# Performance work log

Hardware: AMD Instinct MI355X
Metric: run time of the kernel (lower is better)

## Reference

```python
import jax, jax.numpy as jnp
import numpy as np

A = 15                    # num_anchor_per_point
H = W = 34                # hardcoded feature map size in the torch module
STRIDE = 16               # heat_map_a
ANCHOR_W = jnp.array([45.3, 32.0, 22.6, 90.5, 64.0, 45.3, 181.0, 128.0, 90.5, 271.5, 192.0, 135.8, 362.0, 256.0, 181.0], dtype=jnp.float32)
ANCHOR_H = jnp.array([22.6, 32.0, 45.3, 45.3, 64.0, 90.5, 90.5, 128.0, 181.0, 135.8, 192.0, 271.5, 181.0, 256.0, 362.0], dtype=jnp.float32)
THRESH_OBJ = 0.2
MIN_H = 6.0
MIN_W = 6.0
MAX_CAND = 5000
TOP_N = 300
OVERLAP = 0.7


def _generate_anchors():
    xmins = -0.5 * (ANCHOR_W - 1.0)
    xmaxs = 0.5 * (ANCHOR_W - 1.0)
    ymins = -0.5 * (ANCHOR_H - 1.0)
    ymaxs = 0.5 * (ANCHOR_H - 1.0)
    return jnp.stack([xmins, ymins, xmaxs, ymaxs], axis=1)  # [A,4]


def _bbox_transform_inv(boxes, deltas):
    widths = boxes[:, 2] - boxes[:, 0] + 1.0
    heights = boxes[:, 3] - boxes[:, 1] + 1.0
    ctr_x = boxes[:, 0] + 0.5 * (widths - 1.0)
    ctr_y = boxes[:, 1] + 0.5 * (heights - 1.0)
    pred_ctr_x = deltas[:, 0] * widths + ctr_x
    pred_ctr_y = deltas[:, 1] * heights + ctr_y
    pred_w = jnp.exp(deltas[:, 2]) * widths
    pred_h = jnp.exp(deltas[:, 3]) * heights
    return jnp.stack([
        pred_ctr_x - 0.5 * (pred_w - 1.0),
        pred_ctr_y - 0.5 * (pred_h - 1.0),
        pred_ctr_x + 0.5 * (pred_w - 1.0),
        pred_ctr_y + 0.5 * (pred_h - 1.0),
    ], axis=1)


def _nms_keep(boxes, valid, thresh):
    # greedy NMS on score-descending boxes; +1 pixel convention matches module
    x1, y1, x2, y2 = boxes[:, 0], boxes[:, 1], boxes[:, 2], boxes[:, 3]
    areas = (x2 - x1 + 1.0) * (y2 - y1 + 1.0)
    iw = jnp.clip(jnp.minimum(x2[:, None], x2[None, :]) - jnp.maximum(x1[:, None], x1[None, :]) + 1.0, 0.0)
    ih = jnp.clip(jnp.minimum(y2[:, None], y2[None, :]) - jnp.maximum(y1[:, None], y1[None, :]) + 1.0, 0.0)
    inter = iw * ih
    iou = inter / (areas[:, None] + areas[None, :] - inter)  # [M,M]
    M = boxes.shape[0]
    idx = jnp.arange(M)

    def body(i, suppressed):
        alive = jnp.logical_not(suppressed[i])
        return suppressed | (alive & (iou[i] > thresh) & (idx > i))

    suppressed = jax.lax.fori_loop(0, M, body, jnp.logical_not(valid))
    return jnp.logical_not(suppressed) & valid


def _forward(rpn_cls_prob_reshape, rpn_bbox_pred, im_info, bbox_mean, bbox_std):
    origin_height = im_info[0].astype(jnp.float32)
    origin_width = im_info[1].astype(jnp.float32)

    # shifts (replicates torch meshgrid indexing='ij' and (y,x,y,x) column order)
    shift_x = jnp.arange(W, dtype=jnp.float32) * STRIDE
    shift_y = jnp.arange(H, dtype=jnp.float32) * STRIDE
    sx, sy = jnp.meshgrid(shift_x, shift_y, indexing='ij')  # [W,H]
    shifts = jnp.stack([sy.ravel(), sx.ravel(), sy.ravel(), sx.ravel()], axis=1)  # [W*H,4]
    anchors = (_generate_anchors()[None, :, :] + shifts[:, None, :]).reshape(-1, 4)  # [W*H*A,4]

    # deltas: [1,4A,34,34] -> (A,4,34,34) -> (34,34,A,4) -> (-1,4)
    deltas = rpn_bbox_pred.reshape(A, 4, H, W).transpose(2, 3, 0, 1).reshape(-1, 4)
    deltas = deltas * bbox_std + bbox_mean
    proposals = _bbox_transform_inv(anchors, deltas)

    # clip to image (refine_out_of_map_bbox=True)
    xs = jnp.clip(proposals[:, 0::2], 0.0, origin_width - 1.0)
    ys = jnp.clip(proposals[:, 1::2], 0.0, origin_height - 1.0)
    proposals = jnp.stack([xs[:, 0], ys[:, 0], xs[:, 1], ys[:, 1]], axis=1)

    # scores: [1,2A,34,34] -> (2,A,HW) -> (HW,A,2) -> (-1,2)
    scores = rpn_cls_prob_reshape.reshape(2, A, -1).transpose(2, 1, 0).reshape(-1, 2)

    # filter (HEIGHT_AND_WIDTH) via masking (jit-friendly, same selected set)
    ws = proposals[:, 2] - proposals[:, 0] + 1.0
    hs = proposals[:, 3] - proposals[:, 1] + 1.0
    keep = (scores[:, 1] > THRESH_OBJ) & (ws >= MIN_W) & (hs >= MIN_H)

    masked_score = jnp.where(keep, scores[:, 1], -1.0)
    top_vals, top_idx = jax.lax.top_k(masked_score, MAX_CAND)  # sorted descending
    cand = proposals[top_idx]
    valid = keep[top_idx]

    kept = _nms_keep(cand, valid, OVERLAP)

    # emit first TOP_N kept boxes in score order, zero-padded, with batch-id col 0
    rank = jnp.cumsum(kept.astype(jnp.int32)) - 1
    dest = jnp.where(kept & (rank < TOP_N), rank, TOP_N)
    out = jnp.zeros((TOP_N + 1, 5), dtype=cand.dtype)
    out = out.at[dest, 1:].set(cand)
    return out[:TOP_N]


def setup_inputs() -> dict:
    key = jax.random.key(0)
    k1, k2 = jax.random.split(key)
    rpn_cls_prob_reshape = jax.random.uniform(k1, (1, 2 * A, H, W), dtype=jnp.float32)
    rpn_bbox_pred = jax.random.normal(k2, (1, 4 * A, H, W), dtype=jnp.float32)
    im_info = jnp.array([544, 544], dtype=jnp.int32)
    bbox_mean = jnp.array([0.0, 0.0, 0.0, 0.0], dtype=jnp.float32)
    bbox_std = jnp.array([0.1, 0.1, 0.2, 0.2], dtype=jnp.float32)
    return {"rpn_cls_prob_reshape": rpn_cls_prob_reshape, "rpn_bbox_pred": rpn_bbox_pred,
            "im_info": im_info, "bbox_mean": bbox_mean, "bbox_std": bbox_std}


def reference(rpn_cls_prob_reshape, rpn_bbox_pred, im_info, bbox_mean, bbox_std):
    return _forward(rpn_cls_prob_reshape, rpn_bbox_pred, im_info, bbox_mean, bbox_std)
```

## Files before the change

kernel.cpp:

```cpp
#include <hip/hip_runtime.h>

#define NA 15
#define GH 34
#define GW 34
#define SP (GH*GW)
#define NB (SP*NA)
#define MAXC 5000
#define TOPN 300
#define NW 80
#define NRALLOC 5056
#define THRESH_OBJ 0.2f
#define NMS_T 0.7f
#define SH 12
#define BLO 0x3E4CCu
#define NBUCK 5120

typedef unsigned long long u64;
typedef unsigned int u32;
struct __align__(16) U2 { u64 x, y; };

__constant__ float c_aw[NA] = {45.3f,32.0f,22.6f,90.5f,64.0f,45.3f,181.0f,128.0f,90.5f,271.5f,192.0f,135.8f,362.0f,256.0f,181.0f};
__constant__ float c_ah[NA] = {22.6f,32.0f,45.3f,45.3f,64.0f,90.5f,90.5f,128.0f,181.0f,135.8f,192.0f,271.5f,181.0f,256.0f,362.0f};

__global__ __launch_bounds__(256) void k_decode(
    const float* __restrict__ cls, const float* __restrict__ pred,
    const int* __restrict__ iminfo, const float* __restrict__ mean,
    const float* __restrict__ stdv, float* __restrict__ boxes,
    u32* __restrict__ sbits, int* __restrict__ hist) {
#pragma clang fp contract(off)
  int r = blockIdx.x * 256 + threadIdx.x;
  if (r >= NB) return;
  int n = r % NA;
  int p = r / NA;
  int w = p % GW;
  int h = p / GW;

  float score = cls[(NA + n) * SP + p];

  float d0 = pred[(n*4+0)*SP + p] * stdv[0] + mean[0];
  float d1 = pred[(n*4+1)*SP + p] * stdv[1] + mean[1];
  float d2 = pred[(n*4+2)*SP + p] * stdv[2] + mean[2];
  float d3 = pred[(n*4+3)*SP + p] * stdv[3] + mean[3];

  float aw = c_aw[n], ah = c_ah[n];
  float sx = (float)(w * 16);
  float sy = (float)(h * 16);
  float xmin = -0.5f * (aw - 1.0f) + sx;
  float ymin = -0.5f * (ah - 1.0f) + sy;
  float xmax =  0.5f * (aw - 1.0f) + sx;
  float ymax =  0.5f * (ah - 1.0f) + sy;

  float widths  = xmax - xmin + 1.0f;
  float heights = ymax - ymin + 1.0f;
  float ctrx = xmin + 0.5f * (widths - 1.0f);
  float ctry = ymin + 0.5f * (heights - 1.0f);

  float pcx = d0 * widths + ctrx;
  float pcy = d1 * heights + ctry;
  float pw = expf(d2) * widths;
  float ph = expf(d3) * heights;

  float x1 = pcx - 0.5f * (pw - 1.0f);
  float y1 = pcy - 0.5f * (ph - 1.0f);
  float x2 = pcx + 0.5f * (pw - 1.0f);
  float y2 = pcy + 0.5f * (ph - 1.0f);

  float ow = (float)iminfo[1] - 1.0f;
  float oh = (float)iminfo[0] - 1.0f;
  x1 = fminf(fmaxf(x1, 0.0f), ow);
  x2 = fminf(fmaxf(x2, 0.0f), ow);
  y1 = fminf(fmaxf(y1, 0.0f), oh);
  y2 = fminf(fmaxf(y2, 0.0f), oh);

  float ws = x2 - x1 + 1.0f;
  float hs = y2 - y1 + 1.0f;
  bool keep = (score > THRESH_OBJ) && (ws >= 6.0f) && (hs >= 6.0f);

  boxes[r*4+0] = x1;
  boxes[r*4+1] = y1;
  boxes[r*4+2] = x2;
  boxes[r*4+3] = y2;
  u32 bits = keep ? __float_as_uint(score) : 0u;
  sbits[r] = bits;
  if (bits) {
    int b = min((int)((bits >> SH) - BLO), NBUCK - 1);
    atomicAdd(&hist[b], 1);
  }
}

__global__ __launch_bounds__(1024) void k_scan(const int* __restrict__ hist,
    int* __restrict__ base, int* __restrict__ cnt) {
  __shared__ int sh[NBUCK];
  __shared__ int ch[1024];
  int tid = threadIdx.x;
  for (int j = tid; j < NBUCK; j += 1024) sh[j] = hist[j];
  __syncthreads();
  int c0 = sh[tid*5+0], c1 = sh[tid*5+1], c2 = sh[tid*5+2], c3 = sh[tid*5+3], c4 = sh[tid*5+4];
  ch[tid] = c0 + c1 + c2 + c3 + c4;
  __syncthreads();
  for (int off = 1; off < 1024; off <<= 1) {
    int v = ch[tid];
    int u = (tid + off < 1024) ? ch[tid + off] : 0;
    __syncthreads();
    ch[tid] = v + u;
    __syncthreads();
  }
  int S = (tid + 1 < 1024) ? ch[tid + 1] : 0;
  int b4 = S;
  int b3 = b4 + c4;
  int b2 = b3 + c3;
  int b1 = b2 + c2;
  int b0 = b1 + c1;
  base[tid*5+0] = b0; base[tid*5+1] = b1; base[tid*5+2] = b2;
  base[tid*5+3] = b3; base[tid*5+4] = b4;
  if (tid == 0) *cnt = ch[0];
}

__global__ __launch_bounds__(256) void k_place(const u32* __restrict__ sbits,
    const int* __restrict__ base, int* __restrict__ fill, u64* __restrict__ blist) {
  int i = blockIdx.x * 256 + threadIdx.x;
  if (i >= NB) return;
  u32 bits = sbits[i];
  if (!bits) return;
  int b = min((int)((bits >> SH) - BLO), NBUCK - 1);
  int pos = base[b] + atomicAdd(&fill[b], 1);
  blist[pos] = ((u64)bits << 32) | (u64)(0xFFFFFFFFu - (u32)i);
}

__global__ __launch_bounds__(256) void k_final(const u32* __restrict__ sbits,
    const int* __restrict__ base, const int* __restrict__ cnt,
    const u64* __restrict__ blist, const float* __restrict__ boxes,
    float* __restrict__ sboxes) {
  int i = blockIdx.x * 256 + threadIdx.x;
  if (i >= NB) return;
  u32 bits = sbits[i];
  if (!bits) return;
  int b = min((int)((bits >> SH) - BLO), NBUCK - 1);
  u64 key = ((u64)bits << 32) | (u64)(0xFFFFFFFFu - (u32)i);
  int s = base[b];
  int e = (b > 0) ? base[b-1] : *cnt;
  int r = s;
  for (int p = s; p < e; ++p) r += (blist[p] > key) ? 1 : 0;
  if (r < MAXC) ((float4*)sboxes)[r] = ((const float4*)boxes)[i];
}

__global__ __launch_bounds__(64) void k_iou(const float* __restrict__ sboxes,
    const int* __restrict__ cnt, u64* __restrict__ mask, u64* __restrict__ diag) {
#pragma clang fp contract(off)
  int N = min(*cnt, MAXC);
  int bi = blockIdx.x, bj = blockIdx.y;
  int t = threadIdx.x;
  int i = bi * 64 + t;
  if (bj < bi) {
    if (i < N) mask[(size_t)i * NW + bj] = 0ULL;
    return;
  }
  if (bi * 64 >= N) return;
  __shared__ float4 jb[64];
  int j0 = bj * 64;
  if (j0 + t < N) jb[t] = ((const float4*)sboxes)[j0 + t];
  __syncthreads();
  if (i >= N) return;
  float4 a = ((const float4*)sboxes)[i];
  float areaA = (a.z - a.x + 1.0f) * (a.w - a.y + 1.0f);
  u64 word = 0;
  int jmax = min(64, N - j0);
  for (int jj = 0; jj < jmax; ++jj) {
    int j = j0 + jj;
    if (j <= i) continue;
    float4 b = jb[jj];
    float iw = fminf(a.z, b.z) - fmaxf(a.x, b.x) + 1.0f;
    float ih = fminf(a.w, b.w) - fmaxf(a.y, b.y) + 1.0f;
    iw = fmaxf(iw, 0.0f);
    ih = fmaxf(ih, 0.0f);
    float inter = iw * ih;
    float areaB = (b.z - b.x + 1.0f) * (b.w - b.y + 1.0f);
    float iou = inter / (areaA + areaB - inter);
    if (iou > NMS_T) word |= (1ULL << jj);
  }
  mask[(size_t)i * NW + bj] = word;
  if (bi == bj) diag[i] = word;
}

__device__ __forceinline__ u64 rl64(u64 v, int l) {
  unsigned lo = __builtin_amdgcn_readlane((unsigned)(v & 0xffffffffULL), l);
  unsigned hi = __builtin_amdgcn_readlane((unsigned)(v >> 32), l);
  return ((u64)hi << 32) | (u64)lo;
}

__device__ __forceinline__ void gload_lds16(const void* g, void* l) {
  __builtin_amdgcn_global_load_lds(
      (const __attribute__((address_space(1))) unsigned int*)g,
      (__attribute__((address_space(3))) unsigned int*)l, 16, 0, 0);
}

__global__ __launch_bounds__(64, 1) void k_nms(const float* __restrict__ sboxes,
    const u64* __restrict__ mask, const u64* __restrict__ diag,
    const int* __restrict__ cnt, float* __restrict__ out) {
  const int t = threadIdx.x;
  const int N = min(*cnt, MAXC);
  const int NBLK = (N + 63) >> 6;
  const int tt = (t < 40) ? t : 39;
  const bool lane_ok = (t < 40);
  u64 rv0 = 0ULL, rv1 = 0ULL;
  __shared__ int klist[TOPN + 1];
  __shared__ __align__(16) u64 ring[13 * 128];
  int kept = 0;

  u64 colA = 0ULL, colB = 0ULL;
  if (NBLK > 0) colA = diag[t];
  int pslot = 0;

#define FLUSHRING(n_) do { \
    asm volatile("s_waitcnt vmcnt(0)" ::: "memory"); \
    __builtin_amdgcn_sched_barrier(0); \
    int nf = (n_); \
    U2 q0  = *(const U2*)(ring + 0*128  + 2*tt); \
    U2 q1  = *(const U2*)(ring + 1*128  + 2*tt); \
    U2 q2  = *(const U2*)(ring + 2*128  + 2*tt); \
    U2 q3  = *(const U2*)(ring + 3*128  + 2*tt); \
    U2 q4  = *(const U2*)(ring + 4*128  + 2*tt); \
    U2 q5  = *(const U2*)(ring + 5*128  + 2*tt); \
    U2 q6  = *(const U2*)(ring + 6*128  + 2*tt); \
    U2 q7  = *(const U2*)(ring + 7*128  + 2*tt); \
    U2 q8  = *(const U2*)(ring + 8*128  + 2*tt); \
    U2 q9  = *(const U2*)(ring + 9*128  + 2*tt); \
    U2 q10 = *(const U2*)(ring + 10*128 + 2*tt); \
    U2 q11 = *(const U2*)(ring + 11*128 + 2*tt); \
    u64 o0 = 0, o1 = 0; \
    o0 |= (lane_ok && nf > 0)  ? q0.x  : 0ULL;  o1 |= (lane_ok && nf > 0)  ? q0.y  : 0ULL; \
    o0 |= (lane_ok && nf > 1)  ? q1.x  : 0ULL;  o1 |= (lane_ok && nf > 1)  ? q1.y  : 0ULL; \
    o0 |= (lane_ok && nf > 2)  ? q2.x  : 0ULL;  o1 |= (lane_ok && nf > 2)  ? q2.y  : 0ULL; \
    o0 |= (lane_ok && nf > 3)  ? q3.x  : 0ULL;  o1 |= (lane_ok && nf > 3)  ? q3.y  : 0ULL; \
    o0 |= (lane_ok && nf > 4)  ? q4.x  : 0ULL;  o1 |= (lane_ok && nf > 4)  ? q4.y  : 0ULL; \
    o0 |= (lane_ok && nf > 5)  ? q5.x  : 0ULL;  o1 |= (lane_ok && nf > 5)  ? q5.y  : 0ULL; \
    o0 |= (lane_ok && nf > 6)  ? q6.x  : 0ULL;  o1 |= (lane_ok && nf > 6)  ? q6.y  : 0ULL; \
    o0 |= (lane_ok && nf > 7)  ? q7.x  : 0ULL;  o1 |= (lane_ok && nf > 7)  ? q7.y  : 0ULL; \
    o0 |= (lane_ok && nf > 8)  ? q8.x  : 0ULL;  o1 |= (lane_ok && nf > 8)  ? q8.y  : 0ULL; \
    o0 |= (lane_ok && nf > 9)  ? q9.x  : 0ULL;  o1 |= (lane_ok && nf > 9)  ? q9.y  : 0ULL; \
    o0 |= (lane_ok && nf > 10) ? q10.x : 0ULL;  o1 |= (lane_ok && nf > 10) ? q10.y : 0ULL; \
    o0 |= (lane_ok && nf > 11) ? q11.x : 0ULL;  o1 |= (lane_ok && nf > 11) ? q11.y : 0ULL; \
    rv0 |= o0; rv1 |= o1; \
  } while (0)

  for (int b = 0; b < NBLK; ++b) {
    u64 cc = (b & 1) ? colB : colA;
    if (pslot > 0) { FLUSHRING(pslot); pslot = 0; }
    int base = b * 64;
    u64 w = rl64((b & 1) ? rv1 : rv0, b >> 1);
    int nv = N - base; if (nv > 64) nv = 64;
    u64 valid = (nv >= 64) ? ~0ULL : ((1ULL << nv) - 1ULL);
    u64 avail = ~w & valid;
    if (b + 1 < NBLK) {
      u64 nx = diag[(b + 1) * 64 + t];
      if (b & 1) colA = nx; else colB = nx;
    }
    int slot = 0;
    while (avail && kept < TOPN) {
#pragma unroll
      for (int u = 0; u < 4; ++u) {
        bool on = (avail != 0ULL) && (kept < TOPN);
        int d = (int)__builtin_ctzll(avail | (1ULL << 63));
        int row = base + d;
        klist[on ? kept : TOPN] = row;
        gload_lds16((const char*)(mask + (size_t)row * NW) + (size_t)tt * 16,
                    (void*)(ring + (size_t)(on ? slot : 12) * 128));
        u64 sup = rl64(cc, d);
        u64 clear = on ? (sup | (1ULL << d)) : 0ULL;
        avail &= ~clear;
        kept += on ? 1 : 0;
        slot += on ? 1 : 0;
      }
      if (slot >= 8) { FLUSHRING(slot); slot = 0; }
    }
    if (kept >= TOPN) break;
    pslot = slot;
  }
  __syncthreads();
  for (int e = t; e < TOPN * 5; e += 64) {
    int row = e / 5, col = e % 5;
    float v = 0.0f;
    if (col > 0 && row < kept) v = sboxes[klist[row] * 4 + (col - 1)];
    out[e] = v;
  }
#undef FLUSHRING
}

extern "C" void kernel_launch(void* const* d_in, const int* in_sizes, int n_in,
                              void* d_out, int out_size, void* d_ws, size_t ws_size,
                              hipStream_t stream) {
  const float* cls  = (const float*)d_in[0];
  const float* pred = (const float*)d_in[1];
  const int*   imi  = (const int*)d_in[2];
  const float* mean = (const float*)d_in[3];
  const float* stdv = (const float*)d_in[4];
  float* out = (float*)d_out;

  char* ws = (char*)d_ws;
  float* boxes  = (float*)(ws);
  u32*   sbits  = (u32*)(ws + 277440);
  float* sboxes = (float*)(ws + 346800);
  int*   cnt    = (int*)(ws + 426800);
  int*   hist   = (int*)(ws + 426816);
  int*   fill   = (int*)(ws + 447296);
  int*   base   = (int*)(ws + 467776);
  u64*   mask   = (u64*)(ws + 488256);
  u64*   blist  = mask;
  u64*   diag   = (u64*)(ws + 426816);

  hipMemsetAsync(hist, 0, 2 * NBUCK * sizeof(int), stream);

  k_decode<<<(NB + 255) / 256, 256, 0, stream>>>(cls, pred, imi, mean, stdv, boxes, sbits, hist);
  k_scan<<<1, 1024, 0, stream>>>(hist, base, cnt);
  k_place<<<(NB + 255) / 256, 256, 0, stream>>>(sbits, base, fill, blist);
  k_final<<<(NB + 255) / 256, 256, 0, stream>>>(sbits, base, cnt, blist, boxes, sboxes);
  dim3 giou((MAXC + 63) / 64, NW);
  k_iou<<<giou, 64, 0, stream>>>(sboxes, cnt, mask, diag);
  k_nms<<<1, 64, 0, stream>>>(sboxes, mask, diag, cnt, out);
}
```

Before: 95.01 us.

## Process NMS in 256-row superblocks with register-resident 4-level column masks

The IoU kernel now stores the diagonal plus the next three block-column mask words per row into a compact col4 array, which reuses the start of the workspace (the old boxes buffer, already consumed). The single-wave NMS walks 256-row superblocks. Suppression inside the superblock is propagated through lane reads of register-held words, so the LDS ring is flushed less often (16 slots instead of 8, and once per superblock instead of once per 64-row block). The aim is to cut the serial waitcnt and flush latency on the greedy critical path, at the cost of more registers, more prefetch loads, and extra readlanes per kept box.

```diff
diff --git a/kernel.cpp b/kernel.cpp
--- a/kernel.cpp
+++ b/kernel.cpp
@@ -145,7 +145,7 @@
 }
 
 __global__ __launch_bounds__(64) void k_iou(const float* __restrict__ sboxes,
-    const int* __restrict__ cnt, u64* __restrict__ mask, u64* __restrict__ diag) {
+    const int* __restrict__ cnt, u64* __restrict__ mask, u64* __restrict__ col4) {
 #pragma clang fp contract(off)
   int N = min(*cnt, MAXC);
   int bi = blockIdx.x, bj = blockIdx.y;
@@ -179,7 +179,8 @@
     if (iou > NMS_T) word |= (1ULL << jj);
   }
   mask[(size_t)i * NW + bj] = word;
-  if (bi == bj) diag[i] = word;
+  int lvl = bj - bi;
+  if (lvl < 4) col4[(size_t)i * 4 + lvl] = word;
 }
 
 __device__ __forceinline__ u64 rl64(u64 v, int l) {
@@ -195,21 +196,19 @@
 }
 
 __global__ __launch_bounds__(64, 1) void k_nms(const float* __restrict__ sboxes,
-    const u64* __restrict__ mask, const u64* __restrict__ diag,
+    const u64* __restrict__ mask, const u64* __restrict__ col4,
     const int* __restrict__ cnt, float* __restrict__ out) {
   const int t = threadIdx.x;
   const int N = min(*cnt, MAXC);
   const int NBLK = (N + 63) >> 6;
+  const int NSTEP = (NBLK + 3) >> 2;
   const int tt = (t < 40) ? t : 39;
   const bool lane_ok = (t < 40);
   u64 rv0 = 0ULL, rv1 = 0ULL;
   __shared__ int klist[TOPN + 1];
-  __shared__ __align__(16) u64 ring[13 * 128];
+  __shared__ __align__(16) u64 ring[16 * 128];
   int kept = 0;
-
-  u64 colA = 0ULL, colB = 0ULL;
-  if (NBLK > 0) colA = diag[t];
-  int pslot = 0;
+  int slot = 0;
 
 #define FLUSHRING(n_) do { \
     asm volatile("s_waitcnt vmcnt(0)" ::: "memory"); \
@@ -227,6 +226,10 @@
     U2 q9  = *(const U2*)(ring + 9*128  + 2*tt); \
     U2 q10 = *(const U2*)(ring + 10*128 + 2*tt); \
     U2 q11 = *(const U2*)(ring + 11*128 + 2*tt); \
+    U2 q12 = *(const U2*)(ring + 12*128 + 2*tt); \
+    U2 q13 = *(const U2*)(ring + 13*128 + 2*tt); \
+    U2 q14 = *(const U2*)(ring + 14*128 + 2*tt); \
+    U2 q15 = *(const U2*)(ring + 15*128 + 2*tt); \
     u64 o0 = 0, o1 = 0; \
     o0 |= (lane_ok && nf > 0)  ? q0.x  : 0ULL;  o1 |= (lane_ok && nf > 0)  ? q0.y  : 0ULL; \
     o0 |= (lane_ok && nf > 1)  ? q1.x  : 0ULL;  o1 |= (lane_ok && nf > 1)  ? q1.y  : 0ULL; \
@@ -240,42 +243,71 @@
     o0 |= (lane_ok && nf > 9)  ? q9.x  : 0ULL;  o1 |= (lane_ok && nf > 9)  ? q9.y  : 0ULL; \
     o0 |= (lane_ok && nf > 10) ? q10.x : 0ULL;  o1 |= (lane_ok && nf > 10) ? q10.y : 0ULL; \
     o0 |= (lane_ok && nf > 11) ? q11.x : 0ULL;  o1 |= (lane_ok && nf > 11) ? q11.y : 0ULL; \
+    o0 |= (lane_ok && nf > 12) ? q12.x : 0ULL;  o1 |= (lane_ok && nf > 12) ? q12.y : 0ULL; \
+    o0 |= (lane_ok && nf > 13) ? q13.x : 0ULL;  o1 |= (lane_ok && nf > 13) ? q13.y : 0ULL; \
+    o0 |= (lane_ok && nf > 14) ? q14.x : 0ULL;  o1 |= (lane_ok && nf > 14) ? q14.y : 0ULL; \
+    o0 |= (lane_ok && nf > 15) ? q15.x : 0ULL;  o1 |= (lane_ok && nf > 15) ? q15.y : 0ULL; \
     rv0 |= o0; rv1 |= o1; \
   } while (0)
 
-  for (int b = 0; b < NBLK; ++b) {
-    u64 cc = (b & 1) ? colB : colA;
-    if (pslot > 0) { FLUSHRING(pslot); pslot = 0; }
-    int base = b * 64;
-    u64 w = rl64((b & 1) ? rv1 : rv0, b >> 1);
-    int nv = N - base; if (nv > 64) nv = 64;
-    u64 valid = (nv >= 64) ? ~0ULL : ((1ULL << nv) - 1ULL);
-    u64 avail = ~w & valid;
-    if (b + 1 < NBLK) {
-      u64 nx = diag[(b + 1) * 64 + t];
-      if (b & 1) colA = nx; else colB = nx;
+#define PHASE(P, AV, CSAME, PENDSTMTS) \
+    while (AV) { \
+      int d = (int)__builtin_ctzll(AV); \
+      int row = sb + ((P) << 6) + d; \
+      klist[kept] = row; \
+      gload_lds16((const char*)(mask + (size_t)row * NW) + (size_t)tt * 16, \
+                  (void*)(ring + (size_t)slot * 128)); \
+      AV &= ~(rl64(CSAME, d) | (1ULL << d)); \
+      PENDSTMTS \
+      ++kept; ++slot; \
+      if (kept >= TOPN) goto scan_done; \
+      if (slot == 16) { FLUSHRING(16); slot = 0; } \
     }
-    int slot = 0;
-    while (avail && kept < TOPN) {
-#pragma unroll
-      for (int u = 0; u < 4; ++u) {
-        bool on = (avail != 0ULL) && (kept < TOPN);
-        int d = (int)__builtin_ctzll(avail | (1ULL << 63));
-        int row = base + d;
-        klist[on ? kept : TOPN] = row;
-        gload_lds16((const char*)(mask + (size_t)row * NW) + (size_t)tt * 16,
-                    (void*)(ring + (size_t)(on ? slot : 12) * 128));
-        u64 sup = rl64(cc, d);
-        u64 clear = on ? (sup | (1ULL << d)) : 0ULL;
-        avail &= ~clear;
-        kept += on ? 1 : 0;
-        slot += on ? 1 : 0;
-      }
-      if (slot >= 8) { FLUSHRING(slot); slot = 0; }
+
+  U2 n0a, n0b, n1a, n1b, n2a, n3a;
+  if (NSTEP > 0) {
+    n0a = *(const U2*)(col4 + (size_t)(0*64 + t) * 4);
+    n0b = *(const U2*)(col4 + (size_t)(0*64 + t) * 4 + 2);
+    n1a = *(const U2*)(col4 + (size_t)(1*64 + t) * 4);
+    n1b = *(const U2*)(col4 + (size_t)(1*64 + t) * 4 + 2);
+    n2a = *(const U2*)(col4 + (size_t)(2*64 + t) * 4);
+    n3a = *(const U2*)(col4 + (size_t)(3*64 + t) * 4);
+  }
+
+  for (int s = 0; s < NSTEP; ++s) {
+    const int sb = s * 256, wb = s * 4;
+    if (slot > 0) { FLUSHRING(slot); slot = 0; }
+    u64 c00 = n0a.x, c01 = n0a.y, c02 = n0b.x, c03 = n0b.y;
+    u64 c11 = n1a.x, c12 = n1a.y, c13 = n1b.x;
+    u64 c22 = n2a.x, c23 = n2a.y;
+    u64 c33 = n3a.x;
+    if (s + 1 < NSTEP) {
+      int nb = sb + 256;
+      n0a = *(const U2*)(col4 + (size_t)(nb + 0*64 + t) * 4);
+      n0b = *(const U2*)(col4 + (size_t)(nb + 0*64 + t) * 4 + 2);
+      n1a = *(const U2*)(col4 + (size_t)(nb + 1*64 + t) * 4);
+      n1b = *(const U2*)(col4 + (size_t)(nb + 1*64 + t) * 4 + 2);
+      n2a = *(const U2*)(col4 + (size_t)(nb + 2*64 + t) * 4);
+      n3a = *(const U2*)(col4 + (size_t)(nb + 3*64 + t) * 4);
     }
-    if (kept >= TOPN) break;
-    pslot = slot;
-  }
+    u64 av0, av1, av2, av3;
+#define CARRY(K, dst) { int wi = wb + (K); \
+      u64 w = rl64((wi & 1) ? rv1 : rv0, wi >> 1); \
+      int rem = N - (wi << 6); \
+      u64 vm = (rem >= 64) ? ~0ULL : ((rem <= 0) ? 0ULL : ((1ULL << rem) - 1ULL)); \
+      dst = ~w & vm; }
+    CARRY(0, av0) CARRY(1, av1) CARRY(2, av2) CARRY(3, av3)
+#undef CARRY
+    u64 p1 = 0, p2 = 0, p3 = 0;
+    PHASE(0, av0, c00, p1 |= rl64(c01, d); p2 |= rl64(c02, d); p3 |= rl64(c03, d);)
+    av1 &= ~p1;
+    PHASE(1, av1, c11, p2 |= rl64(c12, d); p3 |= rl64(c13, d);)
+    av2 &= ~p2;
+    PHASE(2, av2, c22, p3 |= rl64(c23, d);)
+    av3 &= ~p3;
+    PHASE(3, av3, c33, ;)
+  }
+scan_done:
   __syncthreads();
   for (int e = t; e < TOPN * 5; e += 64) {
     int row = e / 5, col = e % 5;
@@ -283,6 +315,7 @@
     if (col > 0 && row < kept) v = sboxes[klist[row] * 4 + (col - 1)];
     out[e] = v;
   }
+#undef PHASE
 #undef FLUSHRING
 }
 
@@ -306,7 +339,7 @@
   int*   base   = (int*)(ws + 467776);
   u64*   mask   = (u64*)(ws + 488256);
   u64*   blist  = mask;
-  u64*   diag   = (u64*)(ws + 426816);
+  u64*   col4   = (u64*)ws;
 
   hipMemsetAsync(hist, 0, 2 * NBUCK * sizeof(int), stream);
 
@@ -315,6 +348,6 @@
   k_place<<<(NB + 255) / 256, 256, 0, stream>>>(sbits, base, fill, blist);
   k_final<<<(NB + 255) / 256, 256, 0, stream>>>(sbits, base, cnt, blist, boxes, sboxes);
   dim3 giou((MAXC + 63) / 64, NW);
-  k_iou<<<giou, 64, 0, stream>>>(sboxes, cnt, mask, diag);
-  k_nms<<<1, 64, 0, stream>>>(sboxes, mask, diag, cnt, out);
-}
+  k_iou<<<giou, 64, 0, stream>>>(sboxes, cnt, mask, col4);
+  k_nms<<<1, 64, 0, stream>>>(sboxes, mask, col4, cnt, out);
+}
```

New measurement: 101.5 us. 1.07x slower.

## Drop memset by building histogram in scan kernel; parallelize NMS output emission

Applied to the files above, without the earlier changes.

The histogram is no longer built with global atomics in the decode kernel. The single-block scan kernel now reads all score bits and builds it with shared-memory atomics, and it also zeroes the fill counters, so the separate memset launch goes away. The NMS kernel stops keeping a kept-row list. It enlarges the LDS ring so flushes happen less often, then derives the kept set from the final suppression bitmask and writes output rows in parallel using a wave prefix sum. The cost is a serial pass over about 17k entries in one block for the histogram.

```diff
diff --git a/kernel.cpp b/kernel.cpp
--- a/kernel.cpp
+++ b/kernel.cpp
@@ -26,7 +26,7 @@
     const float* __restrict__ cls, const float* __restrict__ pred,
     const int* __restrict__ iminfo, const float* __restrict__ mean,
     const float* __restrict__ stdv, float* __restrict__ boxes,
-    u32* __restrict__ sbits, int* __restrict__ hist) {
+    u32* __restrict__ sbits) {
 #pragma clang fp contract(off)
   int r = blockIdx.x * 256 + threadIdx.x;
   if (r >= NB) return;
@@ -80,20 +80,20 @@
   boxes[r*4+1] = y1;
   boxes[r*4+2] = x2;
   boxes[r*4+3] = y2;
-  u32 bits = keep ? __float_as_uint(score) : 0u;
-  sbits[r] = bits;
-  if (bits) {
-    int b = min((int)((bits >> SH) - BLO), NBUCK - 1);
-    atomicAdd(&hist[b], 1);
-  }
-}
-
-__global__ __launch_bounds__(1024) void k_scan(const int* __restrict__ hist,
-    int* __restrict__ base, int* __restrict__ cnt) {
+  sbits[r] = keep ? __float_as_uint(score) : 0u;
+}
+
+__global__ __launch_bounds__(1024) void k_scan(const u32* __restrict__ sbits,
+    int* __restrict__ base, int* __restrict__ cnt, int* __restrict__ fill) {
   __shared__ int sh[NBUCK];
   __shared__ int ch[1024];
   int tid = threadIdx.x;
-  for (int j = tid; j < NBUCK; j += 1024) sh[j] = hist[j];
+  for (int j = tid; j < NBUCK; j += 1024) { sh[j] = 0; fill[j] = 0; }
+  __syncthreads();
+  for (int j = tid; j < NB; j += 1024) {
+    u32 bits = sbits[j];
+    if (bits) { int b = min((int)((bits >> SH) - BLO), NBUCK - 1); atomicAdd(&sh[b], 1); }
+  }
   __syncthreads();
   int c0 = sh[tid*5+0], c1 = sh[tid*5+1], c2 = sh[tid*5+2], c3 = sh[tid*5+3], c4 = sh[tid*5+4];
   ch[tid] = c0 + c1 + c2 + c3 + c4;
@@ -202,14 +202,15 @@
   const int NBLK = (N + 63) >> 6;
   const int tt = (t < 40) ? t : 39;
   const bool lane_ok = (t < 40);
+  const int w0i = 2 * tt, w1i = 2 * tt + 1;
   u64 rv0 = 0ULL, rv1 = 0ULL;
-  __shared__ int klist[TOPN + 1];
-  __shared__ __align__(16) u64 ring[13 * 128];
-  int kept = 0;
+  __shared__ __align__(16) u64 ring[17 * 128];
+  int kept = 0, slot = 0;
+
+  const char* mbase = (const char*)mask + (size_t)tt * 16;
 
   u64 colA = 0ULL, colB = 0ULL;
   if (NBLK > 0) colA = diag[t];
-  int pslot = 0;
 
 #define FLUSHRING(n_) do { \
     asm volatile("s_waitcnt vmcnt(0)" ::: "memory"); \
@@ -227,6 +228,10 @@
     U2 q9  = *(const U2*)(ring + 9*128  + 2*tt); \
     U2 q10 = *(const U2*)(ring + 10*128 + 2*tt); \
     U2 q11 = *(const U2*)(ring + 11*128 + 2*tt); \
+    U2 q12 = *(const U2*)(ring + 12*128 + 2*tt); \
+    U2 q13 = *(const U2*)(ring + 13*128 + 2*tt); \
+    U2 q14 = *(const U2*)(ring + 14*128 + 2*tt); \
+    U2 q15 = *(const U2*)(ring + 15*128 + 2*tt); \
     u64 o0 = 0, o1 = 0; \
     o0 |= (lane_ok && nf > 0)  ? q0.x  : 0ULL;  o1 |= (lane_ok && nf > 0)  ? q0.y  : 0ULL; \
     o0 |= (lane_ok && nf > 1)  ? q1.x  : 0ULL;  o1 |= (lane_ok && nf > 1)  ? q1.y  : 0ULL; \
@@ -240,12 +245,16 @@
     o0 |= (lane_ok && nf > 9)  ? q9.x  : 0ULL;  o1 |= (lane_ok && nf > 9)  ? q9.y  : 0ULL; \
     o0 |= (lane_ok && nf > 10) ? q10.x : 0ULL;  o1 |= (lane_ok && nf > 10) ? q10.y : 0ULL; \
     o0 |= (lane_ok && nf > 11) ? q11.x : 0ULL;  o1 |= (lane_ok && nf > 11) ? q11.y : 0ULL; \
+    o0 |= (lane_ok && nf > 12) ? q12.x : 0ULL;  o1 |= (lane_ok && nf > 12) ? q12.y : 0ULL; \
+    o0 |= (lane_ok && nf > 13) ? q13.x : 0ULL;  o1 |= (lane_ok && nf > 13) ? q13.y : 0ULL; \
+    o0 |= (lane_ok && nf > 14) ? q14.x : 0ULL;  o1 |= (lane_ok && nf > 14) ? q14.y : 0ULL; \
+    o0 |= (lane_ok && nf > 15) ? q15.x : 0ULL;  o1 |= (lane_ok && nf > 15) ? q15.y : 0ULL; \
     rv0 |= o0; rv1 |= o1; \
   } while (0)
 
   for (int b = 0; b < NBLK; ++b) {
     u64 cc = (b & 1) ? colB : colA;
-    if (pslot > 0) { FLUSHRING(pslot); pslot = 0; }
+    if (slot > 0) { FLUSHRING(slot); slot = 0; }
     int base = b * 64;
     u64 w = rl64((b & 1) ? rv1 : rv0, b >> 1);
     int nv = N - base; if (nv > 64) nv = 64;
@@ -255,33 +264,70 @@
       u64 nx = diag[(b + 1) * 64 + t];
       if (b & 1) colA = nx; else colB = nx;
     }
-    int slot = 0;
     while (avail && kept < TOPN) {
 #pragma unroll
       for (int u = 0; u < 4; ++u) {
-        bool on = (avail != 0ULL) && (kept < TOPN);
-        int d = (int)__builtin_ctzll(avail | (1ULL << 63));
+        bool on = (avail != 0ULL);
+        int d = (int)__builtin_ctzll(avail | 0x8000000000000000ULL);
         int row = base + d;
-        klist[on ? kept : TOPN] = row;
-        gload_lds16((const char*)(mask + (size_t)row * NW) + (size_t)tt * 16,
-                    (void*)(ring + (size_t)(on ? slot : 12) * 128));
+        gload_lds16(mbase + (size_t)row * (NW * 8),
+                    (void*)(ring + (size_t)(on ? slot : 16) * 128));
         u64 sup = rl64(cc, d);
-        u64 clear = on ? (sup | (1ULL << d)) : 0ULL;
-        avail &= ~clear;
+        avail &= ~(on ? (sup | (1ULL << d)) : 0ULL);
         kept += on ? 1 : 0;
         slot += on ? 1 : 0;
       }
-      if (slot >= 8) { FLUSHRING(slot); slot = 0; }
+      if (slot > 12) { FLUSHRING(slot); slot = 0; }
     }
     if (kept >= TOPN) break;
-    pslot = slot;
-  }
-  __syncthreads();
-  for (int e = t; e < TOPN * 5; e += 64) {
-    int row = e / 5, col = e % 5;
-    float v = 0.0f;
-    if (col > 0 && row < kept) v = sboxes[klist[row] * 4 + (col - 1)];
-    out[e] = v;
+  }
+  if (slot > 0) { FLUSHRING(slot); slot = 0; }
+
+  u64 k0 = 0ULL, k1 = 0ULL;
+  if (lane_ok) {
+    int rem0 = N - w0i * 64;
+    u64 vm0 = (rem0 >= 64) ? ~0ULL : ((rem0 <= 0) ? 0ULL : ((1ULL << rem0) - 1ULL));
+    int rem1 = N - w1i * 64;
+    u64 vm1 = (rem1 >= 64) ? ~0ULL : ((rem1 <= 0) ? 0ULL : ((1ULL << rem1) - 1ULL));
+    k0 = vm0 & ~rv0;
+    k1 = vm1 & ~rv1;
+  }
+  int c0 = __popcll(k0), c1 = __popcll(k1);
+  int c = c0 + c1;
+  int P = c;
+  for (int off = 1; off < 64; off <<= 1) {
+    int v = __shfl_up(P, off, 64);
+    if (t >= off) P += v;
+  }
+  int total = __shfl(P, 63, 64);
+  int excl = P - c;
+  int kout = min(total, TOPN);
+  for (int e = kout * 5 + t; e < TOPN * 5; e += 64) out[e] = 0.0f;
+  int p0 = excl;
+  while (k0) {
+    int d = (int)__builtin_ctzll(k0); k0 &= k0 - 1ULL;
+    if (p0 < kout) {
+      int row = w0i * 64 + d;
+      out[p0*5+0] = 0.0f;
+      out[p0*5+1] = sboxes[row*4+0];
+      out[p0*5+2] = sboxes[row*4+1];
+      out[p0*5+3] = sboxes[row*4+2];
+      out[p0*5+4] = sboxes[row*4+3];
+    }
+    ++p0;
+  }
+  int p1 = excl + c0;
+  while (k1) {
+    int d = (int)__builtin_ctzll(k1); k1 &= k1 - 1ULL;
+    if (p1 < kout) {
+      int row = w1i * 64 + d;
+      out[p1*5+0] = 0.0f;
+      out[p1*5+1] = sboxes[row*4+0];
+      out[p1*5+2] = sboxes[row*4+1];
+      out[p1*5+3] = sboxes[row*4+2];
+      out[p1*5+4] = sboxes[row*4+3];
+    }
+    ++p1;
   }
 #undef FLUSHRING
 }
@@ -301,17 +347,14 @@
   u32*   sbits  = (u32*)(ws + 277440);
   float* sboxes = (float*)(ws + 346800);
   int*   cnt    = (int*)(ws + 426800);
-  int*   hist   = (int*)(ws + 426816);
   int*   fill   = (int*)(ws + 447296);
   int*   base   = (int*)(ws + 467776);
   u64*   mask   = (u64*)(ws + 488256);
   u64*   blist  = mask;
   u64*   diag   = (u64*)(ws + 426816);
 
-  hipMemsetAsync(hist, 0, 2 * NBUCK * sizeof(int), stream);
-
-  k_decode<<<(NB + 255) / 256, 256, 0, stream>>>(cls, pred, imi, mean, stdv, boxes, sbits, hist);
-  k_scan<<<1, 1024, 0, stream>>>(hist, base, cnt);
+  k_decode<<<(NB + 255) / 256, 256, 0, stream>>>(cls, pred, imi, mean, stdv, boxes, sbits);
+  k_scan<<<1, 1024, 0, stream>>>(sbits, base, cnt, fill);
   k_place<<<(NB + 255) / 256, 256, 0, stream>>>(sbits, base, fill, blist);
   k_final<<<(NB + 255) / 256, 256, 0, stream>>>(sbits, base, cnt, blist, boxes, sboxes);
   dim3 giou((MAXC + 63) / 64, NW);
```

After: 100.4 us. +5.7%, slower.

## Build score histogram in scan kernel LDS and prefetch NMS mask via helper waves

Applied to the files above, without the earlier changes.

The global histogram atomics and the memset are removed from the decode kernel. The single-block scan kernel now builds the histogram itself with shared-memory atomics over all sbits, and it also zeros the fill array. The NMS kernel launches with three extra waves that stream the mask and diag arrays through the cache, so the serial wave's dependent loads are more likely to hit. In exchange, one block now does a serial pass over about 17k entries, and the helper waves compete with the NMS wave for memory bandwidth.

```diff
diff --git a/kernel.cpp b/kernel.cpp
--- a/kernel.cpp
+++ b/kernel.cpp
@@ -26,7 +26,7 @@
     const float* __restrict__ cls, const float* __restrict__ pred,
     const int* __restrict__ iminfo, const float* __restrict__ mean,
     const float* __restrict__ stdv, float* __restrict__ boxes,
-    u32* __restrict__ sbits, int* __restrict__ hist) {
+    u32* __restrict__ sbits) {
 #pragma clang fp contract(off)
   int r = blockIdx.x * 256 + threadIdx.x;
   if (r >= NB) return;
@@ -80,20 +80,20 @@
   boxes[r*4+1] = y1;
   boxes[r*4+2] = x2;
   boxes[r*4+3] = y2;
-  u32 bits = keep ? __float_as_uint(score) : 0u;
-  sbits[r] = bits;
-  if (bits) {
-    int b = min((int)((bits >> SH) - BLO), NBUCK - 1);
-    atomicAdd(&hist[b], 1);
-  }
-}
-
-__global__ __launch_bounds__(1024) void k_scan(const int* __restrict__ hist,
-    int* __restrict__ base, int* __restrict__ cnt) {
+  sbits[r] = keep ? __float_as_uint(score) : 0u;
+}
+
+__global__ __launch_bounds__(1024) void k_scan(const u32* __restrict__ sbits,
+    int* __restrict__ base, int* __restrict__ cnt, int* __restrict__ fill) {
   __shared__ int sh[NBUCK];
   __shared__ int ch[1024];
   int tid = threadIdx.x;
-  for (int j = tid; j < NBUCK; j += 1024) sh[j] = hist[j];
+  for (int j = tid; j < NBUCK; j += 1024) { sh[j] = 0; fill[j] = 0; }
+  __syncthreads();
+  for (int j = tid; j < NB; j += 1024) {
+    u32 bits = sbits[j];
+    if (bits) { int b = min((int)((bits >> SH) - BLO), NBUCK - 1); atomicAdd(&sh[b], 1); }
+  }
   __syncthreads();
   int c0 = sh[tid*5+0], c1 = sh[tid*5+1], c2 = sh[tid*5+2], c3 = sh[tid*5+3], c4 = sh[tid*5+4];
   ch[tid] = c0 + c1 + c2 + c3 + c4;
@@ -194,22 +194,46 @@
       (__attribute__((address_space(3))) unsigned int*)l, 16, 0, 0);
 }
 
-__global__ __launch_bounds__(64, 1) void k_nms(const float* __restrict__ sboxes,
+__global__ __launch_bounds__(256, 1) void k_nms(const float* __restrict__ sboxes,
     const u64* __restrict__ mask, const u64* __restrict__ diag,
     const int* __restrict__ cnt, float* __restrict__ out) {
-  const int t = threadIdx.x;
+  const int tid = threadIdx.x;
+  const int wv = tid >> 6;
+  const int t = tid & 63;
   const int N = min(*cnt, MAXC);
+  __shared__ int klist[TOPN + 1];
+  __shared__ __align__(16) u64 ring[13 * 128];
+  __shared__ int s_kept;
+
+  if (wv > 0) {
+    float acc = 0.0f;
+    if (wv == 1) {
+      const float4* d4 = (const float4*)diag;
+      for (int i = t; i < 2528; i += 64) {
+        float4 v = d4[i];
+        acc += v.x + v.y + v.z + v.w;
+      }
+    }
+    const float4* m4 = (const float4*)mask;
+    size_t total = (size_t)N * 40;
+    for (size_t i = (size_t)(wv - 1) * 64 + t; i < total; i += 192) {
+      float4 v = m4[i];
+      acc += v.x + v.y + v.z + v.w;
+    }
+    asm volatile("" :: "v"(acc));
+    __syncthreads();
+    return;
+  }
+
   const int NBLK = (N + 63) >> 6;
   const int tt = (t < 40) ? t : 39;
   const bool lane_ok = (t < 40);
   u64 rv0 = 0ULL, rv1 = 0ULL;
-  __shared__ int klist[TOPN + 1];
-  __shared__ __align__(16) u64 ring[13 * 128];
   int kept = 0;
 
   u64 colA = 0ULL, colB = 0ULL;
   if (NBLK > 0) colA = diag[t];
-  int pslot = 0;
+  int slot = 0;
 
 #define FLUSHRING(n_) do { \
     asm volatile("s_waitcnt vmcnt(0)" ::: "memory"); \
@@ -245,7 +269,7 @@
 
   for (int b = 0; b < NBLK; ++b) {
     u64 cc = (b & 1) ? colB : colA;
-    if (pslot > 0) { FLUSHRING(pslot); pslot = 0; }
+    if (slot > 0) { FLUSHRING(slot); slot = 0; }
     int base = b * 64;
     u64 w = rl64((b & 1) ? rv1 : rv0, b >> 1);
     int nv = N - base; if (nv > 64) nv = 64;
@@ -255,7 +279,6 @@
       u64 nx = diag[(b + 1) * 64 + t];
       if (b & 1) colA = nx; else colB = nx;
     }
-    int slot = 0;
     while (avail && kept < TOPN) {
 #pragma unroll
       for (int u = 0; u < 4; ++u) {
@@ -274,9 +297,10 @@
       if (slot >= 8) { FLUSHRING(slot); slot = 0; }
     }
     if (kept >= TOPN) break;
-    pslot = slot;
-  }
-  __syncthreads();
+  }
+  if (t == 0) s_kept = kept;
+  __syncthreads();
+  kept = s_kept;
   for (int e = t; e < TOPN * 5; e += 64) {
     int row = e / 5, col = e % 5;
     float v = 0.0f;
@@ -301,20 +325,17 @@
   u32*   sbits  = (u32*)(ws + 277440);
   float* sboxes = (float*)(ws + 346800);
   int*   cnt    = (int*)(ws + 426800);
-  int*   hist   = (int*)(ws + 426816);
   int*   fill   = (int*)(ws + 447296);
   int*   base   = (int*)(ws + 467776);
   u64*   mask   = (u64*)(ws + 488256);
   u64*   blist  = mask;
   u64*   diag   = (u64*)(ws + 426816);
 
-  hipMemsetAsync(hist, 0, 2 * NBUCK * sizeof(int), stream);
-
-  k_decode<<<(NB + 255) / 256, 256, 0, stream>>>(cls, pred, imi, mean, stdv, boxes, sbits, hist);
-  k_scan<<<1, 1024, 0, stream>>>(hist, base, cnt);
+  k_decode<<<(NB + 255) / 256, 256, 0, stream>>>(cls, pred, imi, mean, stdv, boxes, sbits);
+  k_scan<<<1, 1024, 0, stream>>>(sbits, base, cnt, fill);
   k_place<<<(NB + 255) / 256, 256, 0, stream>>>(sbits, base, fill, blist);
   k_final<<<(NB + 255) / 256, 256, 0, stream>>>(sbits, base, cnt, blist, boxes, sboxes);
   dim3 giou((MAXC + 63) / 64, NW);
   k_iou<<<giou, 64, 0, stream>>>(sboxes, cnt, mask, diag);
-  k_nms<<<1, 64, 0, stream>>>(sboxes, mask, diag, cnt, out);
-}
+  k_nms<<<1, 256, 0, stream>>>(sboxes, mask, diag, cnt, out);
+}
```

After: 344.7 us. +262.9%, slower.
